# Kernel tuning notes

Hardware: AMD Instinct MI355X
Metric: run time of the kernel (lower is better)

The kernel has to match this reference:

```python
import jax, jax.numpy as jnp
import numpy as np

N, L, V, D, E, NL = 50000, 32, 5000, 128, 800000, 3
P, B = 5000, 64

def setup_inputs() -> dict:
    key = jax.random.key(0)
    ks = jax.random.split(key, 6)
    x = jax.random.randint(ks[0], (N, L), 0, V)            # token ids, 0 = pad
    edge_index = jax.random.randint(ks[1], (2, E), 0, N)   # [2,E] src,dst
    pool_idx = jnp.arange(N) // (N // P)                   # node -> pooled supernode
    node_batch = pool_idx * B // P                         # node -> graph id (grouped, as in torch loop)
    embed = jax.random.normal(ks[2], (V, D), jnp.float32) * 0.02
    W_l = jax.random.normal(ks[3], (NL, D, D), jnp.float32) / np.sqrt(D)
    W_r = jax.random.normal(ks[4], (NL, D, D), jnp.float32) / np.sqrt(D)
    b = jnp.zeros((NL, D), jnp.float32)
    return dict(x=x, edge_index=edge_index, pool_idx=pool_idx, node_batch=node_batch,
                num_pooled=P, embed=embed, W_l=W_l, W_r=W_r, b=b)

def reference(x, edge_index, pool_idx, node_batch, num_pooled, embed, W_l, W_r, b):
    n = x.shape[0]
    dt = embed.dtype
    # masked mean-pool of token embeddings (pad id = 0), length clamped to >=1
    mask = (x != 0)
    lengths = jnp.clip(mask.sum(axis=1), 1, None).astype(dt)          # [N]
    h = (embed[x] * mask[..., None].astype(dt)).sum(axis=1) / lengths[:, None]  # [N,D]
    src, dst = edge_index[0], edge_index[1]
    deg = jnp.clip(jax.ops.segment_sum(jnp.ones(src.shape[0], dt), dst, num_segments=n), 1.0, None)
    # SAGEConv layers: mean-aggregate neighbors, lin_l(agg)+bias + lin_r(self), relu
    # (dropout p=0.5 is identity in eval mode)
    for i in range(W_l.shape[0]):
        agg = jax.ops.segment_sum(h[src], dst, num_segments=n) / deg[:, None]
        h = jax.nn.relu(agg @ W_l[i] + b[i] + h @ W_r[i])
    # global mean pool over supernodes
    cnt = jnp.clip(jax.ops.segment_sum(jnp.ones(n, dt), pool_idx, num_segments=num_pooled), 1.0, None)
    x_pooled = jax.ops.segment_sum(h, pool_idx, num_segments=num_pooled) / cnt[:, None]
    # global max pool of graph ids -> pooled batch vector
    batch_pooled = jax.ops.segment_max(node_batch, pool_idx, num_segments=num_pooled)
    # coalesced pooled edges without self-loops, as a dense boolean adjacency
    sp, dp = pool_idx[src], pool_idx[dst]
    adj = jnp.zeros((num_pooled, num_pooled), jnp.bool_).at[sp, dp].set(True)
    adj = adj & ~jnp.eye(num_pooled, dtype=jnp.bool_)
    return x_pooled, adj, batch_pooled
```

## Files before the change

### kernel.cpp

```cpp
#include <hip/hip_runtime.h>
#include <hip/hip_fp16.h>
#include <limits.h>

#define D 128
#define NBK 768
#define EB  2048
#define SCL 64.0f

typedef __attribute__((ext_vector_type(8))) short bf16x8;
typedef __attribute__((ext_vector_type(4))) float f32x4;
typedef __attribute__((ext_vector_type(2))) float f32x2;

#if __has_builtin(__builtin_amdgcn_cvt_pk_f32_fp8) && __has_builtin(__builtin_amdgcn_cvt_pk_fp8_f32)
#define HW_FP8 1
#endif

static __device__ __forceinline__ unsigned short f2bf(float f) {
    unsigned u = __builtin_bit_cast(unsigned, f);
    u += 0x7FFFu + ((u >> 16) & 1u);
    return (unsigned short)(u >> 16);
}
static __device__ __forceinline__ float bf2f(unsigned u16) {
    unsigned u = u16 << 16;
    return __builtin_bit_cast(float, u);
}
static __device__ __forceinline__ bf16x8 load_frag(const unsigned short* p) {
    uint4 v = *(const uint4*)p;
    return __builtin_bit_cast(bf16x8, v);
}
static __device__ __forceinline__ ushort4 pack4(const float* a, float s) {
    ushort4 o;
    o.x = f2bf(a[0] * s); o.y = f2bf(a[1] * s);
    o.z = f2bf(a[2] * s); o.w = f2bf(a[3] * s);
    return o;
}

static __device__ __forceinline__ unsigned char f2q(float v) {
#ifdef HW_FP8
    return (unsigned char)(__builtin_amdgcn_cvt_pk_fp8_f32(v, v, 0, false) & 0xff);
#else
    unsigned short u = __half_as_ushort(__float2half(v));
    u = (unsigned short)(u + 0x7F + ((u >> 8) & 1));
    return (unsigned char)(u >> 8);
#endif
}
static __device__ __forceinline__ unsigned enc4(float a0, float a1, float a2, float a3) {
#ifdef HW_FP8
    unsigned u = __builtin_amdgcn_cvt_pk_fp8_f32(a0, a1, 0, false);
    u = __builtin_amdgcn_cvt_pk_fp8_f32(a2, a3, (int)u, true);
    return u;
#else
    return (unsigned)f2q(a0) | ((unsigned)f2q(a1) << 8) |
           ((unsigned)f2q(a2) << 16) | ((unsigned)f2q(a3) << 24);
#endif
}
static __device__ __forceinline__ void dec4(float* a, unsigned u) {
#ifdef HW_FP8
    f32x2 lo = __builtin_amdgcn_cvt_pk_f32_fp8((int)u, false);
    f32x2 hi = __builtin_amdgcn_cvt_pk_f32_fp8((int)u, true);
    a[0] += lo.x; a[1] += lo.y; a[2] += hi.x; a[3] += hi.y;
#else
    a[0] += __half2float(__ushort_as_half((unsigned short)((u & 0xff) << 8)));
    a[1] += __half2float(__ushort_as_half((unsigned short)(((u >> 8) & 0xff) << 8)));
    a[2] += __half2float(__ushort_as_half((unsigned short)(((u >> 16) & 0xff) << 8)));
    a[3] += __half2float(__ushort_as_half((unsigned short)((u >> 24) << 8)));
#endif
}
static __device__ __forceinline__ void dec16(float* a, uint4 v) {
    dec4(a, v.x); dec4(a + 4, v.y); dec4(a + 8, v.z); dec4(a + 12, v.w);
}

__global__ __launch_bounds__(256) void zero_k(float4* __restrict__ b, size_t nb)
{
    size_t i = (size_t)blockIdx.x * 256 + threadIdx.x;
    if (i < nb) b[i] = make_float4(0.f, 0.f, 0.f, 0.f);
}

__global__ __launch_bounds__(256) void epack_k(
    const float* __restrict__ embed, unsigned* __restrict__ e8, int n4)
{
    int i = blockIdx.x * 256 + threadIdx.x;
    if (i >= n4) return;
    float4 v = *(const float4*)&embed[(size_t)i * 4];
    e8[i] = enc4(v.x * SCL, v.y * SCL, v.z * SCL, v.w * SCL);
}

__global__ __launch_bounds__(256) void embed_pool_k(
    const int* __restrict__ x, const unsigned char* __restrict__ e8,
    unsigned short* __restrict__ h16, unsigned char* __restrict__ h8, int n, int L)
{
    __shared__ int toks[16][32];
    int t = threadIdx.x;
    int sub = t >> 4, s = t & 15;
    int node = blockIdx.x * 16 + sub;
    for (int j = t; j < 16 * L; j += 256) {
        int nd = blockIdx.x * 16 + j / L;
        toks[j / L][j % L] = (nd < n) ? x[(size_t)nd * L + (j % L)] : 0;
    }
    __syncthreads();
    if (node >= n) return;
    float acc[8] = {};
    int cnt = 0;
    for (int l = 0; l < L; ++l) {
        int tok = toks[sub][l];
        if (tok != 0) {
            uint2 v = *(const uint2*)&e8[(size_t)tok * D + s * 8];
            dec4(acc, v.x); dec4(acc + 4, v.y);
            cnt++;
        }
    }
    float c = (float)(cnt > 0 ? cnt : 1);
    float invh = 1.0f / (SCL * c);
    float inv8 = 1.0f / c;
    ushort4 lo = pack4(acc, invh), hi = pack4(acc + 4, invh);
    *(ushort4*)&h16[(size_t)node * D + s * 8]     = lo;
    *(ushort4*)&h16[(size_t)node * D + s * 8 + 4] = hi;
    uint2 q;
    q.x = enc4(acc[0] * inv8, acc[1] * inv8, acc[2] * inv8, acc[3] * inv8);
    q.y = enc4(acc[4] * inv8, acc[5] * inv8, acc[6] * inv8, acc[7] * inv8);
    *(uint2*)&h8[(size_t)node * D + s * 8] = q;
}

__global__ __launch_bounds__(256) void wpack_k(
    const float* __restrict__ Wl, const float* __restrict__ Wr,
    unsigned short* __restrict__ Wp, int NL)
{
    int idx = blockIdx.x * 256 + threadIdx.x;
    if (idx >= NL * 2 * 16384) return;
    int m = idx >> 14;
    int r = idx & 16383;
    int j = r & 7;
    int lane = (r >> 3) & 63;
    int cb = (r >> 9) & 7;
    int kb = (r >> 12) & 3;
    const float* W = ((m & 1) ? Wr : Wl) + (size_t)(m >> 1) * D * D;
    int k = kb * 32 + (lane >> 4) * 8 + j;
    int c = cb * 16 + (lane & 15);
    Wp[idx] = f2bf(W[(size_t)k * D + c]);
}

__global__ __launch_bounds__(256) void deghist_k(
    const int* __restrict__ ei, const int* __restrict__ pool,
    int* __restrict__ degall, int E, int n, int P, int nblk)
{
    __shared__ int hist[NBK];
    int t = threadIdx.x;
    for (int i = t; i < NBK; i += 256) hist[i] = 0;
    __syncthreads();
    int base = blockIdx.x * EB;
    int lim = min(E, base + EB);
    for (int e = base + t; e < lim; e += 256) {
        int src = ei[e], dst = ei[E + e];
        atomicAdd(&degall[dst], 1);
        int sp = pool[src], dp = pool[dst];
        if (sp != dp) atomicAdd(&hist[(sp * P + dp) >> 15], 1);
    }
    __syncthreads();
    for (int i = t; i < NBK; i += 256)
        degall[n + i * nblk + blockIdx.x] = hist[i];
}

__global__ __launch_bounds__(256) void scan_partial_k(
    const int* __restrict__ deg, int* __restrict__ bsum, int n)
{
    int b = blockIdx.x, t = threadIdx.x;
    int i0 = b * 1024 + t * 4;
    int s = 0;
    #pragma unroll
    for (int k = 0; k < 4; ++k) { int i = i0 + k; if (i < n) s += deg[i]; }
    for (int off = 32; off > 0; off >>= 1) s += __shfl_down(s, off, 64);
    __shared__ int sm4[4];
    if ((t & 63) == 0) sm4[t >> 6] = s;
    __syncthreads();
    if (t == 0) bsum[b] = sm4[0] + sm4[1] + sm4[2] + sm4[3];
}

__global__ __launch_bounds__(512) void scan_bsum_k(
    const int* __restrict__ bsum, int* __restrict__ boff, int nb)
{
    __shared__ int sm[512];
    int t = threadIdx.x;
    sm[t] = (t < nb) ? bsum[t] : 0;
    __syncthreads();
    for (int off = 1; off < 512; off <<= 1) {
        int add = (t >= off) ? sm[t - off] : 0;
        __syncthreads();
        sm[t] += add;
        __syncthreads();
    }
    if (t < nb) boff[t] = (t > 0) ? sm[t - 1] : 0;
}

__global__ __launch_bounds__(256) void scan_final_k(
    const int* __restrict__ deg, const int* __restrict__ boff,
    int* __restrict__ rp, int n)
{
    __shared__ int sm[256];
    int b = blockIdx.x, t = threadIdx.x;
    int i0 = b * 1024 + t * 4;
    int v[4];
    #pragma unroll
    for (int k = 0; k < 4; ++k) { int i = i0 + k; v[k] = (i < n) ? deg[i] : 0; }
    v[1] += v[0]; v[2] += v[1]; v[3] += v[2];
    sm[t] = v[3];
    __syncthreads();
    for (int off = 1; off < 256; off <<= 1) {
        int add = (t >= off) ? sm[t - off] : 0;
        __syncthreads();
        sm[t] += add;
        __syncthreads();
    }
    int base = boff[b] + ((t > 0) ? sm[t - 1] : 0);
    if (b == 0 && t == 0) rp[0] = 0;
    #pragma unroll
    for (int k = 0; k < 4; ++k) {
        int i = i0 + k;
        if (i < n) rp[i + 1] = base + v[k];
    }
}

__global__ __launch_bounds__(256) void csr_scatter_k(
    const int* __restrict__ ei, const int* __restrict__ rpall,
    int* __restrict__ cur, int* __restrict__ col, int E)
{
    int e = blockIdx.x * 256 + threadIdx.x;
    if (e >= E) return;
    int src = ei[e], dst = ei[E + e];
    int pos = atomicAdd(&cur[dst], 1);
    col[rpall[dst] + pos] = src;
}

__global__ __launch_bounds__(256) void bkt_scatter_k(
    const int* __restrict__ ei, const int* __restrict__ rpall,
    const int* __restrict__ pool, int* __restrict__ kbuf,
    int E, int n, int P, int nblk)
{
    __shared__ int off[NBK];
    int t = threadIdx.x;
    for (int i = t; i < NBK; i += 256)
        off[i] = rpall[n + i * nblk + blockIdx.x] - E;
    __syncthreads();
    int base = blockIdx.x * EB;
    int lim = min(E, base + EB);
    for (int e = base + t; e < lim; e += 256) {
        int src = ei[e], dst = ei[E + e];
        int sp = pool[src], dp = pool[dst];
        if (sp != dp) {
            int key = sp * P + dp;
            int kpos = atomicAdd(&off[key >> 15], 1);
            kbuf[kpos] = key;
        }
    }
}

__global__ __launch_bounds__(256) void adj_write_k(
    const int* __restrict__ rpall, const int* __restrict__ kbuf,
    float* __restrict__ adj, int E, int n, int nblk, int ns)
{
    int b = blockIdx.x;
    int s = rpall[n + b * nblk] - E;
    int e = (b == NBK - 1) ? (rpall[ns] - E) : (rpall[n + (b + 1) * nblk] - E);
    for (int i = s + threadIdx.x; i < e; i += 256)
        adj[(size_t)kbuf[i]] = 1.0f;
}

__global__ __launch_bounds__(256) void aggregate_k(
    const unsigned char* __restrict__ h8, const int* __restrict__ rp,
    const int* __restrict__ col, unsigned short* __restrict__ agg16, int n)
{
    int node = blockIdx.x * 4 + (threadIdx.x >> 6);
    int lane = threadIdx.x & 63;
    if (node >= n) return;
    int beg = rp[node], end = rp[node + 1];
    int oct = lane >> 3, s = lane & 7;
    float acc[16] = {};
    int e = beg + oct;
    for (; e + 8 < end; e += 16) {
        uint4 v0 = *(const uint4*)&h8[(size_t)col[e] * D + s * 16];
        uint4 v1 = *(const uint4*)&h8[(size_t)col[e + 8] * D + s * 16];
        dec16(acc, v0);
        dec16(acc, v1);
    }
    if (e < end)
        dec16(acc, *(const uint4*)&h8[(size_t)col[e] * D + s * 16]);
    #pragma unroll
    for (int k = 0; k < 16; ++k) {
        acc[k] += __shfl_xor(acc[k], 8, 64);
        acc[k] += __shfl_xor(acc[k], 16, 64);
        acc[k] += __shfl_xor(acc[k], 32, 64);
    }
    if (oct == 0) {
        int dg = end - beg;
        float inv = 1.0f / (SCL * (float)(dg > 0 ? dg : 1));
        ushort4 o0 = pack4(acc, inv),     o1 = pack4(acc + 4, inv);
        ushort4 o2 = pack4(acc + 8, inv), o3 = pack4(acc + 12, inv);
        *(ushort4*)&agg16[(size_t)node * D + s * 16]      = o0;
        *(ushort4*)&agg16[(size_t)node * D + s * 16 + 4]  = o1;
        *(ushort4*)&agg16[(size_t)node * D + s * 16 + 8]  = o2;
        *(ushort4*)&agg16[(size_t)node * D + s * 16 + 12] = o3;
    }
}

__global__ __launch_bounds__(256) void sage_gemm_mfma_k(
    const unsigned short* __restrict__ agg16, unsigned short* __restrict__ h16,
    unsigned char* __restrict__ h8, const unsigned short* __restrict__ Wp,
    const float* __restrict__ bias, int n, int write8)
{
    int t = threadIdx.x;
    int w = t >> 6, lane = t & 63;
    int node0 = blockIdx.x * 128 + w * 32;
    int row = lane & 15, g = lane >> 4;

    f32x4 acc[2][8];
    #pragma unroll
    for (int i = 0; i < 2; ++i)
        #pragma unroll
        for (int c = 0; c < 8; ++c)
            acc[i][c] = (f32x4){0.f, 0.f, 0.f, 0.f};

    float bs[8];
    #pragma unroll
    for (int cb = 0; cb < 8; ++cb) bs[cb] = bias[cb * 16 + row];

    bool ok0 = (node0 < n);
    bool ok1 = (node0 + 16 < n);

    #pragma unroll
    for (int kb = 0; kb < 8; ++kb) {
        const unsigned short* Asrc = (kb < 4) ? agg16 : h16;
        int ko = (kb & 3) * 32 + g * 8;
        bf16x8 a0 = (bf16x8){0,0,0,0,0,0,0,0};
        bf16x8 a1 = a0;
        if (ok0) a0 = load_frag(&Asrc[(size_t)(node0 + row) * D + ko]);
        if (ok1) a1 = load_frag(&Asrc[(size_t)(node0 + 16 + row) * D + ko]);
        const unsigned short* wp = Wp + ((kb < 4) ? 0 : 16384) + (size_t)(kb & 3) * 4096;
        #pragma unroll
        for (int cb = 0; cb < 8; ++cb) {
            bf16x8 b = load_frag(&wp[(cb * 64 + lane) * 8]);
            acc[0][cb] = __builtin_amdgcn_mfma_f32_16x16x32_bf16(a0, b, acc[0][cb], 0, 0, 0);
            acc[1][cb] = __builtin_amdgcn_mfma_f32_16x16x32_bf16(a1, b, acc[1][cb], 0, 0, 0);
        }
    }

    #pragma unroll
    for (int rg = 0; rg < 2; ++rg) {
        int nb = node0 + rg * 16;
        if (nb >= n) break;
        #pragma unroll
        for (int cb = 0; cb < 8; ++cb) {
            int c = cb * 16 + row;
            #pragma unroll
            for (int j = 0; j < 4; ++j) {
                int node = nb + g * 4 + j;
                float v = fmaxf(acc[rg][cb][j] + bs[cb], 0.f);
                h16[(size_t)node * D + c] = f2bf(v);
                if (write8) h8[(size_t)node * D + c] = f2q(v * SCL);
            }
        }
    }
}

__global__ __launch_bounds__(128) void poolmean_k(
    const unsigned short* __restrict__ h16, const int* __restrict__ pool,
    const int* __restrict__ nbatch, float* __restrict__ outx,
    float* __restrict__ outb, int n, int P)
{
    int p = blockIdx.x;
    int d = threadIdx.x;
    int lo = 0, hi = n;
    while (lo < hi) { int mid = (lo + hi) >> 1; if (pool[mid] < p) lo = mid + 1; else hi = mid; }
    int s = lo;
    hi = n;
    while (lo < hi) { int mid = (lo + hi) >> 1; if (pool[mid] < p + 1) lo = mid + 1; else hi = mid; }
    int e = lo;
    float sum = 0.f;
    for (int i = s; i < e; ++i) sum += bf2f(h16[(size_t)i * D + d]);
    int c = e - s;
    outx[(size_t)p * D + d] = sum / (float)(c > 0 ? c : 1);
    if (d == 0) {
        int bm = INT_MIN;
        for (int i = s; i < e; ++i) bm = max(bm, nbatch[i]);
        outb[p] = (float)bm;
    }
}

extern "C" void kernel_launch(void* const* d_in, const int* in_sizes, int n_in,
                              void* d_out, int out_size, void* d_ws, size_t ws_size,
                              hipStream_t stream)
{
    const int*   x      = (const int*)d_in[0];
    const int*   ei     = (const int*)d_in[1];
    const int*   pool   = (const int*)d_in[2];
    const int*   nbatch = (const int*)d_in[3];
    const float* embed  = (const float*)d_in[5];
    const float* Wl     = (const float*)d_in[6];
    const float* Wr     = (const float*)d_in[7];
    const float* bias   = (const float*)d_in[8];

    const int N  = in_sizes[2];
    const int L  = in_sizes[0] / N;
    const int E  = in_sizes[1] / 2;
    const int VD = in_sizes[5];
    const int NL = in_sizes[6] / (D * D);
    const int P  = 5000;

    float* out_x   = (float*)d_out;
    float* out_adj = out_x + (size_t)P * D;
    float* out_b   = out_adj + (size_t)P * P;

    char* w = (char*)d_ws;
    auto alloc = [&](size_t bytes) { void* p = w; w += (bytes + 255) & ~255ULL; return p; };
    size_t ND = (size_t)N * D;
    unsigned short* h16   = (unsigned short*)alloc(ND * 2);
    unsigned short* agg16 = (unsigned short*)alloc(ND * 2);
    unsigned char*  h8    = (unsigned char*)alloc(ND);
    unsigned short* Wp    = (unsigned short*)alloc((size_t)NL * 2 * 16384 * 2);
    unsigned char*  e8    = (unsigned char*)alloc((size_t)VD);

    const int NBLK = (E + EB - 1) / EB;
    const int NS   = N + NBK * NBLK;
    const int NB   = (NS + 1023) / 1024;

    int*   col    = (int*)alloc((size_t)E * 4);
    int*   kbuf   = (int*)alloc((size_t)E * 4);
    int*   rpall  = (int*)alloc((size_t)(NS + 1) * 4);
    int*   bsum   = (int*)alloc(512 * 4);
    int*   boff   = (int*)alloc(512 * 4);
    int*   degall = (int*)alloc((size_t)(NS + N) * 4);
    int*   cur    = degall + NS;

    size_t nz = ((size_t)(NS + N) + 3) / 4;
    zero_k<<<(int)((nz + 255) / 256), 256, 0, stream>>>((float4*)degall, nz);

    epack_k<<<(VD / 4 + 255) / 256, 256, 0, stream>>>(embed, (unsigned*)e8, VD / 4);
    wpack_k<<<(NL * 2 * 16384 + 255) / 256, 256, 0, stream>>>(Wl, Wr, Wp, NL);
    embed_pool_k<<<(N + 15) / 16, 256, 0, stream>>>(x, e8, h16, h8, N, L);
    deghist_k<<<NBLK, 256, 0, stream>>>(ei, pool, degall, E, N, P, NBLK);
    scan_partial_k<<<NB, 256, 0, stream>>>(degall, bsum, NS);
    scan_bsum_k<<<1, 512, 0, stream>>>(bsum, boff, NB);
    scan_final_k<<<NB, 256, 0, stream>>>(degall, boff, rpall, NS);
    csr_scatter_k<<<(E + 255) / 256, 256, 0, stream>>>(ei, rpall, cur, col, E);
    bkt_scatter_k<<<NBLK, 256, 0, stream>>>(ei, rpall, pool, kbuf, E, N, P, NBLK);
    adj_write_k<<<NBK, 256, 0, stream>>>(rpall, kbuf, out_adj, E, N, NBLK, NS);

    for (int ly = 0; ly < NL; ++ly) {
        aggregate_k<<<(N + 3) / 4, 256, 0, stream>>>(h8, rpall, col, agg16, N);
        sage_gemm_mfma_k<<<(N + 127) / 128, 256, 0, stream>>>(
            agg16, h16, h8, Wp + (size_t)ly * 2 * 16384, bias + (size_t)ly * D, N,
            (ly < NL - 1) ? 1 : 0);
    }

    poolmean_k<<<P, 128, 0, stream>>>(h16, pool, nbatch, out_x, out_b, N, P);
}
```

Measured before the change: 308.9 us.

## Fuse pack kernels, shrink zeroing, unroll embed pool, aggregation and pool-mean loops

```diff
diff --git a/kernel.cpp b/kernel.cpp
--- a/kernel.cpp
+++ b/kernel.cpp
@@ -70,21 +70,41 @@
     dec4(a, v.x); dec4(a + 4, v.y); dec4(a + 8, v.z); dec4(a + 12, v.w);
 }
 
-__global__ __launch_bounds__(256) void zero_k(float4* __restrict__ b, size_t nb)
+__global__ __launch_bounds__(256) void zero_k(
+    float4* __restrict__ a, size_t na, float4* __restrict__ b, size_t nb)
 {
     size_t i = (size_t)blockIdx.x * 256 + threadIdx.x;
-    if (i < nb) b[i] = make_float4(0.f, 0.f, 0.f, 0.f);
-}
-
-__global__ __launch_bounds__(256) void epack_k(
-    const float* __restrict__ embed, unsigned* __restrict__ e8, int n4)
+    float4 z = make_float4(0.f, 0.f, 0.f, 0.f);
+    if (i < na) a[i] = z;
+    else if (i - na < nb) b[i - na] = z;
+}
+
+__global__ __launch_bounds__(256) void pack_k(
+    const float* __restrict__ embed, unsigned* __restrict__ e8, int n4,
+    const float* __restrict__ Wl, const float* __restrict__ Wr,
+    unsigned short* __restrict__ Wp, int NL)
 {
     int i = blockIdx.x * 256 + threadIdx.x;
-    if (i >= n4) return;
-    float4 v = *(const float4*)&embed[(size_t)i * 4];
-    e8[i] = enc4(v.x * SCL, v.y * SCL, v.z * SCL, v.w * SCL);
-}
-
+    if (i < n4) {
+        float4 v = *(const float4*)&embed[(size_t)i * 4];
+        e8[i] = enc4(v.x * SCL, v.y * SCL, v.z * SCL, v.w * SCL);
+    }
+    int idx = i - n4;
+    if (idx >= 0 && idx < NL * 2 * 16384) {
+        int m = idx >> 14;
+        int r = idx & 16383;
+        int j = r & 7;
+        int lane = (r >> 3) & 63;
+        int cb = (r >> 9) & 7;
+        int kb = (r >> 12) & 3;
+        const float* W = ((m & 1) ? Wr : Wl) + (size_t)(m >> 1) * D * D;
+        int k = kb * 32 + (lane >> 4) * 8 + j;
+        int c = cb * 16 + (lane & 15);
+        Wp[idx] = f2bf(W[(size_t)k * D + c]);
+    }
+}
+
+template <int LT>
 __global__ __launch_bounds__(256) void embed_pool_k(
     const int* __restrict__ x, const unsigned char* __restrict__ e8,
     unsigned short* __restrict__ h16, unsigned char* __restrict__ h8, int n, int L)
@@ -93,20 +113,29 @@
     int t = threadIdx.x;
     int sub = t >> 4, s = t & 15;
     int node = blockIdx.x * 16 + sub;
-    for (int j = t; j < 16 * L; j += 256) {
-        int nd = blockIdx.x * 16 + j / L;
-        toks[j / L][j % L] = (nd < n) ? x[(size_t)nd * L + (j % L)] : 0;
+    int LL = LT ? LT : L;
+    for (int j = t; j < 16 * LL; j += 256) {
+        int nd = blockIdx.x * 16 + j / LL;
+        toks[j / LL][j % LL] = (nd < n) ? x[(size_t)nd * LL + (j % LL)] : 0;
     }
     __syncthreads();
     if (node >= n) return;
     float acc[8] = {};
     int cnt = 0;
-    for (int l = 0; l < L; ++l) {
-        int tok = toks[sub][l];
-        if (tok != 0) {
+    #pragma unroll
+    for (int l = 0; l < (LT ? LT : 1); ++l) {
+        int ll = LT ? l : 0;
+        if (!LT) break;
+        int tok = toks[sub][ll];
+        uint2 v = *(const uint2*)&e8[(size_t)tok * D + s * 8];
+        if (tok != 0) { dec4(acc, v.x); dec4(acc + 4, v.y); cnt++; }
+    }
+    if (!LT) {
+        #pragma unroll 8
+        for (int l = 0; l < L; ++l) {
+            int tok = toks[sub][l];
             uint2 v = *(const uint2*)&e8[(size_t)tok * D + s * 8];
-            dec4(acc, v.x); dec4(acc + 4, v.y);
-            cnt++;
+            if (tok != 0) { dec4(acc, v.x); dec4(acc + 4, v.y); cnt++; }
         }
     }
     float c = (float)(cnt > 0 ? cnt : 1);
@@ -121,24 +150,6 @@
     *(uint2*)&h8[(size_t)node * D + s * 8] = q;
 }
 
-__global__ __launch_bounds__(256) void wpack_k(
-    const float* __restrict__ Wl, const float* __restrict__ Wr,
-    unsigned short* __restrict__ Wp, int NL)
-{
-    int idx = blockIdx.x * 256 + threadIdx.x;
-    if (idx >= NL * 2 * 16384) return;
-    int m = idx >> 14;
-    int r = idx & 16383;
-    int j = r & 7;
-    int lane = (r >> 3) & 63;
-    int cb = (r >> 9) & 7;
-    int kb = (r >> 12) & 3;
-    const float* W = ((m & 1) ? Wr : Wl) + (size_t)(m >> 1) * D * D;
-    int k = kb * 32 + (lane >> 4) * 8 + j;
-    int c = cb * 16 + (lane & 15);
-    Wp[idx] = f2bf(W[(size_t)k * D + c]);
-}
-
 __global__ __launch_bounds__(256) void deghist_k(
     const int* __restrict__ ei, const int* __restrict__ pool,
     int* __restrict__ degall, int E, int n, int P, int nblk)
@@ -275,11 +286,19 @@
     int oct = lane >> 3, s = lane & 7;
     float acc[16] = {};
     int e = beg + oct;
+    for (; e + 24 < end; e += 32) {
+        int c0 = col[e], c1 = col[e + 8], c2 = col[e + 16], c3 = col[e + 24];
+        uint4 v0 = *(const uint4*)&h8[(size_t)c0 * D + s * 16];
+        uint4 v1 = *(const uint4*)&h8[(size_t)c1 * D + s * 16];
+        uint4 v2 = *(const uint4*)&h8[(size_t)c2 * D + s * 16];
+        uint4 v3 = *(const uint4*)&h8[(size_t)c3 * D + s * 16];
+        dec16(acc, v0); dec16(acc, v1); dec16(acc, v2); dec16(acc, v3);
+    }
     for (; e + 8 < end; e += 16) {
-        uint4 v0 = *(const uint4*)&h8[(size_t)col[e] * D + s * 16];
-        uint4 v1 = *(const uint4*)&h8[(size_t)col[e + 8] * D + s * 16];
-        dec16(acc, v0);
-        dec16(acc, v1);
+        int c0 = col[e], c1 = col[e + 8];
+        uint4 v0 = *(const uint4*)&h8[(size_t)c0 * D + s * 16];
+        uint4 v1 = *(const uint4*)&h8[(size_t)c1 * D + s * 16];
+        dec16(acc, v0); dec16(acc, v1);
     }
     if (e < end)
         dec16(acc, *(const uint4*)&h8[(size_t)col[e] * D + s * 16]);
@@ -373,13 +392,21 @@
     hi = n;
     while (lo < hi) { int mid = (lo + hi) >> 1; if (pool[mid] < p + 1) lo = mid + 1; else hi = mid; }
     int e = lo;
-    float sum = 0.f;
-    for (int i = s; i < e; ++i) sum += bf2f(h16[(size_t)i * D + d]);
+    float s0 = 0.f, s1 = 0.f, s2 = 0.f, s3 = 0.f;
+    int i = s;
+    for (; i + 3 < e; i += 4) {
+        s0 += bf2f(h16[(size_t)(i + 0) * D + d]);
+        s1 += bf2f(h16[(size_t)(i + 1) * D + d]);
+        s2 += bf2f(h16[(size_t)(i + 2) * D + d]);
+        s3 += bf2f(h16[(size_t)(i + 3) * D + d]);
+    }
+    for (; i < e; ++i) s0 += bf2f(h16[(size_t)i * D + d]);
+    float sum = (s0 + s1) + (s2 + s3);
     int c = e - s;
     outx[(size_t)p * D + d] = sum / (float)(c > 0 ? c : 1);
     if (d == 0) {
         int bm = INT_MIN;
-        for (int i = s; i < e; ++i) bm = max(bm, nbatch[i]);
+        for (int j = s; j < e; ++j) bm = max(bm, nbatch[j]);
         outb[p] = (float)bm;
     }
 }
@@ -426,15 +453,23 @@
     int*   rpall  = (int*)alloc((size_t)(NS + 1) * 4);
     int*   bsum   = (int*)alloc(512 * 4);
     int*   boff   = (int*)alloc(512 * 4);
-    int*   degall = (int*)alloc((size_t)(NS + N) * 4);
-    int*   cur    = degall + NS;
-
-    size_t nz = ((size_t)(NS + N) + 3) / 4;
-    zero_k<<<(int)((nz + 255) / 256), 256, 0, stream>>>((float4*)degall, nz);
-
-    epack_k<<<(VD / 4 + 255) / 256, 256, 0, stream>>>(embed, (unsigned*)e8, VD / 4);
-    wpack_k<<<(NL * 2 * 16384 + 255) / 256, 256, 0, stream>>>(Wl, Wr, Wp, NL);
-    embed_pool_k<<<(N + 15) / 16, 256, 0, stream>>>(x, e8, h16, h8, N, L);
+    int*   degall = (int*)alloc((size_t)NS * 4);
+    int*   cur    = (int*)alloc((size_t)N * 4);
+
+    size_t na = ((size_t)N + 3) / 4;
+    zero_k<<<(int)((na * 2 + 255) / 256), 256, 0, stream>>>(
+        (float4*)degall, na, (float4*)cur, na);
+
+    int n4 = VD / 4;
+    int packtot = n4 + NL * 2 * 16384;
+    pack_k<<<(packtot + 255) / 256, 256, 0, stream>>>(
+        embed, (unsigned*)e8, n4, Wl, Wr, Wp, NL);
+
+    if (L == 32)
+        embed_pool_k<32><<<(N + 15) / 16, 256, 0, stream>>>(x, e8, h16, h8, N, L);
+    else
+        embed_pool_k<0><<<(N + 15) / 16, 256, 0, stream>>>(x, e8, h16, h8, N, L);
+
     deghist_k<<<NBLK, 256, 0, stream>>>(ei, pool, degall, E, N, P, NBLK);
     scan_partial_k<<<NB, 256, 0, stream>>>(degall, bsum, NS);
     scan_bsum_k<<<1, 512, 0, stream>>>(bsum, boff, NB);
```

After: 324.7 us. 5.1% more time.
